# Performance work log

Hardware: AMD Instinct MI355X
Metric: run time of the kernel (lower is better)

## Reference

```python
import jax, jax.numpy as jnp
import numpy as np

H = 1024      # controller hidden size
M = 4096      # memory rows (must equal WORD per original code's buffer shapes)
WORD = 4096   # word size
R = 4         # read heads
NW = 2        # write heads
MODES = 1 + 2 * NW
EPS = 1e-3


def _lin(x, W, b):
    return x @ W.T + b


def _allocation(usage):
    # usage: [1, M] -> allocation weighting via ascending usage sort (DNC)
    u = EPS + (1.0 - EPS) * usage
    order = jnp.argsort(u, axis=1)                       # ascending (least used first)
    sorted_u = jnp.take_along_axis(u, order, axis=1)
    prod = jnp.cumprod(sorted_u, axis=1)
    excl = jnp.concatenate([jnp.ones((1, 1), u.dtype), prod[:, :-1]], axis=1)
    sorted_alloc = (1.0 - sorted_u) * excl
    return jnp.zeros_like(u).at[0, order[0]].set(sorted_alloc[0])


def _dnc_forward(x, memory, prev_read_weights, prev_write_weights, prev_link,
                 prev_precedence, prev_usage,
                 W_wv, b_wv, W_ev, b_ev, W_fg, b_fg, W_ag, b_ag, W_wg, b_wg,
                 W_rm, b_rm, W_wk, b_wk, W_ws, b_ws, W_rk, b_rk, W_rs, b_rs):
    # ---- read_inputs ----
    write_vector = _lin(x, W_wv, b_wv).reshape(NW, WORD)
    erase_vector = jax.nn.sigmoid(_lin(x, W_ev, b_ev)).reshape(NW, WORD)
    free_gate = jax.nn.sigmoid(_lin(x, W_fg, b_fg))          # [1,R]
    allocation_gate = jax.nn.sigmoid(_lin(x, W_ag, b_ag))    # [1,NW]
    write_gate = jax.nn.sigmoid(_lin(x, W_wg, b_wg))         # [1,NW]
    read_mode = jax.nn.sigmoid(_lin(x, W_rm, b_rm)).reshape(R, MODES)
    write_keys = jax.nn.sigmoid(_lin(x, W_wk, b_wk)).reshape(NW, WORD)
    write_strengths = _lin(x, W_ws, b_ws)                    # [1,NW]
    read_keys = _lin(x, W_rk, b_rk).reshape(R, WORD)
    read_strengths = _lin(x, W_rs, b_rs)                     # [1,R]

    # ---- usage ----
    ww_term = 1.0 - jnp.prod(prev_write_weights, axis=1)                   # [1,M]
    usage = prev_usage + (1.0 - prev_usage) * ww_term
    phi = 1.0 - jnp.prod(free_gate[..., None] * prev_read_weights, axis=1)
    usage = usage * phi

    # ---- write weights (cosine content + sequential allocation per head) ----
    dot = jnp.einsum('wd,bmd->bwm', write_keys, memory)                    # [1,NW,M]
    mem_norms = jnp.sqrt(jnp.sum(memory * memory, axis=2))                 # [1,M]
    key_norms = jnp.sqrt(jnp.sum(write_keys * write_keys, axis=1))         # [NW]
    similarity = dot / (key_norms[None, :, None] * mem_norms[:, None, :] + EPS)

    write_gates = (allocation_gate * write_gate)[..., None]                # [1,NW,1]
    ww_rows = []
    for i in range(NW):  # small fixed head loop (sequential usage dependency)
        beta = 1.0 + jax.nn.softplus(write_strengths[0, i])
        cw = jax.nn.softmax(similarity[0, i] * beta)                       # [M]
        a = _allocation(usage)                                             # [1,M]
        usage = usage + (1.0 - usage) * write_gates[:, i, :] * a
        ww_rows.append(write_gate[0, i] * (allocation_gate[0, i] * a[0]
                       + (1.0 - allocation_gate[0, i]) * cw))
    write_weights = jnp.stack(ww_rows)[None]                               # [1,NW,M]

    # ---- erase and write ----
    weighted_resets = write_weights[..., None] * erase_vector[None, :, None, :]
    reset_gate = jnp.prod(1.0 - weighted_resets, axis=1)                   # [1,M,WORD]
    new_memory = memory * reset_gate + jnp.einsum('bwm,wd->bmd', write_weights, write_vector)

    # ---- temporal linkage ----
    wi = write_weights[..., None]          # [1,NW,M,1]
    wj = write_weights[:, :, None, :]      # [1,NW,1,M]
    pj = prev_precedence[:, :, None, :]    # [1,NW,1,M]
    link = (1.0 - wi - wj) * prev_link + wi * pj
    link = link * (1.0 - jnp.eye(M, dtype=link.dtype))
    write_sum = jnp.sum(write_weights, axis=2, keepdims=True)
    precedence = (1.0 - write_sum) * prev_precedence + write_weights

    # ---- read weights ----
    rdot = jnp.einsum('rd,bmd->brm', read_keys, new_memory)
    new_mem_norms = jnp.sqrt(jnp.sum(new_memory * new_memory, axis=2))
    rkey_norms = jnp.sqrt(jnp.sum(read_keys * read_keys, axis=1))
    rsim = rdot / (rkey_norms[None, :, None] * new_mem_norms[:, None, :])  # note: no eps here (as in source)
    content_weights = jax.nn.softmax(rsim * read_strengths[0][None, :, None], axis=-1)

    expanded = jnp.broadcast_to(prev_read_weights[:, None], (1, NW, R, M))  # stack((rw,rw)) with NW=2
    fwd_w = jnp.einsum('bwrm,bwnm->brwn', expanded, link)   # rw @ link^T, permuted -> [1,R,NW,M]
    bwd_w = jnp.einsum('bwrm,bwmn->brwn', expanded, link)   # rw @ link,   permuted -> [1,R,NW,M]
    rm = read_mode[None]                                    # [1,R,MODES]
    backward_mode = rm[:, :, :NW]
    forward_mode = rm[:, :, NW:2 * NW]
    content_mode = rm[:, :, 2 * NW:]                        # [1,R,1]
    read_weights = (jnp.einsum('brw,brwm->brm', backward_mode, bwd_w)
                    + jnp.einsum('brw,brwm->brm', forward_mode, fwd_w)
                    + content_mode * content_weights)
    read_words = jnp.einsum('brm,bmd->brd', read_weights, new_memory)      # [1,R,WORD]
    return read_words, new_memory, read_weights, write_weights, link, precedence, usage


def setup_inputs() -> dict:
    key = jax.random.key(0)
    ks = jax.random.split(key, 32)
    rn = lambda i, s: jax.random.normal(ks[i], s, dtype=jnp.float32)
    ru = lambda i, s: jax.random.uniform(ks[i], s, dtype=jnp.float32)
    w = lambda i, s: rn(i, s) * 0.02
    return {
        'x': rn(0, (1, H)),
        'memory': rn(1, (1, M, WORD)),
        'prev_read_weights': ru(2, (1, R, M)),
        'prev_write_weights': ru(3, (1, NW, M)),
        'prev_link': ru(4, (1, NW, M, M)),
        'prev_precedence': ru(5, (1, NW, M)),
        'prev_usage': ru(6, (1, M)),
        'W_wv': w(7, (NW * WORD, H)), 'b_wv': jnp.zeros((NW * WORD,), jnp.float32),
        'W_ev': w(8, (NW * WORD, H)), 'b_ev': jnp.zeros((NW * WORD,), jnp.float32),
        'W_fg': w(9, (R, H)), 'b_fg': jnp.zeros((R,), jnp.float32),
        'W_ag': w(10, (NW, H)), 'b_ag': jnp.zeros((NW,), jnp.float32),
        'W_wg': w(11, (NW, H)), 'b_wg': jnp.zeros((NW,), jnp.float32),
        'W_rm': w(12, (R * MODES, H)), 'b_rm': jnp.zeros((R * MODES,), jnp.float32),
        'W_wk': w(13, (NW * WORD, H)), 'b_wk': jnp.zeros((NW * WORD,), jnp.float32),
        'W_ws': w(14, (NW, H)), 'b_ws': jnp.zeros((NW,), jnp.float32),
        'W_rk': w(15, (R * WORD, H)), 'b_rk': jnp.zeros((R * WORD,), jnp.float32),
        'W_rs': w(16, (R, H)), 'b_rs': jnp.zeros((R,), jnp.float32),
    }


def reference(x, memory, prev_read_weights, prev_write_weights, prev_link,
              prev_precedence, prev_usage,
              W_wv, b_wv, W_ev, b_ev, W_fg, b_fg, W_ag, b_ag, W_wg, b_wg,
              W_rm, b_rm, W_wk, b_wk, W_ws, b_ws, W_rk, b_rk, W_rs, b_rs):
    return _dnc_forward(x, memory, prev_read_weights, prev_write_weights, prev_link,
                        prev_precedence, prev_usage,
                        W_wv, b_wv, W_ev, b_ev, W_fg, b_fg, W_ag, b_ag, W_wg, b_wg,
                        W_rm, b_rm, W_wk, b_wk, W_ws, b_ws, W_rk, b_rk, W_rs, b_rs)
```

## Files before the change

### kernel.cpp

```cpp
#include <hip/hip_runtime.h>
#include <math.h>

#define HD 1024
#define MD 4096
#define WD 4096
#define RD 4
#define NWD 2
#define MODESD 5
#define EPSF 0.001f

#define O_WORDS 0
#define O_NM    16384
#define O_RW    16793600
#define O_WW    16809984
#define O_LINK  16818176
#define O_PREC  50372608
#define O_USAGE 50380800

#define WS_WV   0
#define WS_EV   8192
#define WS_WK   16384
#define WS_RK   24576
#define WS_FG   40960
#define WS_AG   40976
#define WS_WG   40992
#define WS_RM   41008
#define WS_WSTR 41040
#define WS_RS   41056
#define WS_KN   41072
#define WS_RKN  41088
#define WS_UPRE 41104
#define WS_SIM  45200
#define WS_RDOT 53392
#define WS_NMN  69776
#define WS_CONT 73872
#define WS_FWD  90256
#define WS_BWD  123024

__device__ __forceinline__ float waveReduceSum(float v) {
#pragma unroll
  for (int o = 32; o; o >>= 1) v += __shfl_down(v, o, 64);
  return v;
}

__global__ void gemv_kernel(const float* __restrict__ W, const float* __restrict__ b,
                            const float* __restrict__ x, float* __restrict__ out,
                            int rows, int act) {
  __shared__ float4 xs[HD / 4];
  int t = threadIdx.x;
  const float4* x4 = (const float4*)x;
  xs[t] = x4[t];
  __syncthreads();
  int wave = t >> 6, lane = t & 63;
  int row = blockIdx.x * 4 + wave;
  if (row >= rows) return;
  const float4* W4 = (const float4*)(W + (size_t)row * HD);
  float acc = 0.f;
#pragma unroll
  for (int i = 0; i < 4; ++i) {
    float4 w = W4[i * 64 + lane];
    float4 xv = xs[i * 64 + lane];
    acc += w.x * xv.x + w.y * xv.y + w.z * xv.z + w.w * xv.w;
  }
  acc = waveReduceSum(acc);
  if (lane == 0) {
    float v = acc + b[row];
    if (act) v = 1.f / (1.f + expf(-v));
    out[row] = v;
  }
}

__global__ void norms_kernel(const float* __restrict__ wk, const float* __restrict__ rk,
                             float* __restrict__ kn, float* __restrict__ rkn) {
  int v = blockIdx.x;
  const float* p = (v < 2) ? (wk + v * WD) : (rk + (v - 2) * WD);
  float s = 0.f;
  for (int d = threadIdx.x; d < WD; d += 256) { float t = p[d]; s += t * t; }
  s = waveReduceSum(s);
  __shared__ float sh[4];
  int wave = threadIdx.x >> 6, lane = threadIdx.x & 63;
  if (lane == 0) sh[wave] = s;
  __syncthreads();
  if (threadIdx.x == 0) {
    float r = sqrtf(sh[0] + sh[1] + sh[2] + sh[3]);
    if (v < 2) kn[v] = r; else rkn[v - 2] = r;
  }
}

__global__ void usage_kernel(const float* __restrict__ pusage, const float* __restrict__ pww,
                             const float* __restrict__ prw, const float* __restrict__ fg,
                             float* __restrict__ upre) {
  int m = blockIdx.x * 256 + threadIdx.x;
  float pw = 1.f;
#pragma unroll
  for (int w = 0; w < NWD; ++w) pw *= pww[w * MD + m];
  float pu = pusage[m];
  float u = pu + (1.f - pu) * (1.f - pw);
  float pr = 1.f;
#pragma unroll
  for (int r = 0; r < RD; ++r) pr *= fg[r] * prw[r * MD + m];
  upre[m] = u * (1.f - pr);
}

__global__ void sim_kernel(const float* __restrict__ mem, const float* __restrict__ wk,
                           const float* __restrict__ kn, float* __restrict__ sim) {
  int m = blockIdx.x;
  int t = threadIdx.x;
  const float4* row = (const float4*)(mem + (size_t)m * WD);
  const float4* k0 = (const float4*)wk;
  const float4* k1 = (const float4*)(wk + WD);
  float d0 = 0, d1 = 0, s = 0;
  for (int i = t; i < WD / 4; i += 256) {
    float4 v = row[i], a = k0[i], b = k1[i];
    d0 += v.x * a.x + v.y * a.y + v.z * a.z + v.w * a.w;
    d1 += v.x * b.x + v.y * b.y + v.z * b.z + v.w * b.w;
    s  += v.x * v.x + v.y * v.y + v.z * v.z + v.w * v.w;
  }
  d0 = waveReduceSum(d0); d1 = waveReduceSum(d1); s = waveReduceSum(s);
  __shared__ float sh[3][4];
  int wave = t >> 6, lane = t & 63;
  if (lane == 0) { sh[0][wave] = d0; sh[1][wave] = d1; sh[2][wave] = s; }
  __syncthreads();
  if (t == 0) {
    float D0 = sh[0][0] + sh[0][1] + sh[0][2] + sh[0][3];
    float D1 = sh[1][0] + sh[1][1] + sh[1][2] + sh[1][3];
    float S  = sh[2][0] + sh[2][1] + sh[2][2] + sh[2][3];
    float mn = sqrtf(S);
    sim[0 * MD + m] = D0 / (kn[0] * mn + EPSF);
    sim[1 * MD + m] = D1 / (kn[1] * mn + EPSF);
  }
}

__global__ __launch_bounds__(1024) void ww_kernel(
    const float* __restrict__ sim, const float* __restrict__ upre,
    const float* __restrict__ wstr, const float* __restrict__ ag,
    const float* __restrict__ wg, const float* __restrict__ pprec,
    float* __restrict__ out_ww, float* __restrict__ out_prec,
    float* __restrict__ out_usage) {
  __shared__ float u_s[MD];
  __shared__ float sv[MD];
  __shared__ unsigned short si[MD];
  __shared__ float a_s[MD];
  __shared__ float red[1024];
  int t = threadIdx.x;
  for (int m = t; m < MD; m += 1024) u_s[m] = upre[m];
  __syncthreads();

  for (int head = 0; head < NWD; ++head) {
    float beta = 1.f + log1pf(expf(wstr[head]));
    float agv = ag[head], wgv = wg[head];

    float mx = -3.4e38f;
    for (int m = t; m < MD; m += 1024) mx = fmaxf(mx, sim[head * MD + m] * beta);
    red[t] = mx; __syncthreads();
    for (int s = 512; s; s >>= 1) { if (t < s) red[t] = fmaxf(red[t], red[t + s]); __syncthreads(); }
    mx = red[0]; __syncthreads();
    float sm = 0.f;
    for (int m = t; m < MD; m += 1024) sm += expf(sim[head * MD + m] * beta - mx);
    red[t] = sm; __syncthreads();
    for (int s = 512; s; s >>= 1) { if (t < s) red[t] += red[t + s]; __syncthreads(); }
    float inv = 1.f / red[0]; __syncthreads();

    for (int m = t; m < MD; m += 1024) { sv[m] = EPSF + (1.f - EPSF) * u_s[m]; si[m] = (unsigned short)m; }
    __syncthreads();
    for (int k = 2; k <= MD; k <<= 1) {
      for (int j = k >> 1; j > 0; j >>= 1) {
        for (int i = t; i < MD; i += 1024) {
          int ixj = i ^ j;
          if (ixj > i) {
            float v1 = sv[i], v2 = sv[ixj];
            unsigned short i1 = si[i], i2 = si[ixj];
            bool gt = (v1 > v2) || (v1 == v2 && i1 > i2);
            bool up = ((i & k) == 0);
            if (gt == up) { sv[i] = v2; sv[ixj] = v1; si[i] = i2; si[ixj] = i1; }
          }
        }
        __syncthreads();
      }
    }
    float l0 = sv[t * 4 + 0], l1 = sv[t * 4 + 1], l2 = sv[t * 4 + 2], l3 = sv[t * 4 + 3];
    unsigned short s0 = si[t * 4 + 0], s1 = si[t * 4 + 1], s2 = si[t * 4 + 2], s3 = si[t * 4 + 3];
    red[t] = l0 * l1 * l2 * l3; __syncthreads();
    for (int off = 1; off < 1024; off <<= 1) {
      float val = (t >= off) ? red[t - off] : 1.f;
      __syncthreads();
      red[t] *= val;
      __syncthreads();
    }
    float carry = (t > 0) ? red[t - 1] : 1.f;
    __syncthreads();
    float e0 = carry, e1 = e0 * l0, e2 = e1 * l1, e3 = e2 * l2;
    a_s[s0] = (1.f - l0) * e0;
    a_s[s1] = (1.f - l1) * e1;
    a_s[s2] = (1.f - l2) * e2;
    a_s[s3] = (1.f - l3) * e3;
    __syncthreads();

    float agwg = agv * wgv;
    for (int m = t; m < MD; m += 1024) {
      float cwv = expf(sim[head * MD + m] * beta - mx) * inv;
      float a = a_s[m];
      float uu = u_s[m];
      u_s[m] = uu + (1.f - uu) * agwg * a;
      out_ww[head * MD + m] = wgv * (agv * a + (1.f - agv) * cwv);
    }
    __syncthreads();
  }

  for (int head = 0; head < NWD; ++head) {
    float s = 0.f;
    for (int m = t; m < MD; m += 1024) s += out_ww[head * MD + m];
    red[t] = s; __syncthreads();
    for (int ss = 512; ss; ss >>= 1) { if (t < ss) red[t] += red[t + ss]; __syncthreads(); }
    float wsum = red[0]; __syncthreads();
    for (int m = t; m < MD; m += 1024)
      out_prec[head * MD + m] = (1.f - wsum) * pprec[head * MD + m] + out_ww[head * MD + m];
  }
  for (int m = t; m < MD; m += 1024) out_usage[m] = u_s[m];
}

__global__ void newmem_kernel(const float* __restrict__ mem, const float* __restrict__ ww,
                              const float* __restrict__ ev, const float* __restrict__ wvv,
                              const float* __restrict__ rk, float* __restrict__ nm_out,
                              float* __restrict__ rdot, float* __restrict__ nmn) {
  int m = blockIdx.x;
  int t = threadIdx.x;
  float w0 = ww[m], w1 = ww[MD + m];
  const float4* row = (const float4*)(mem + (size_t)m * WD);
  const float4* e0 = (const float4*)ev;
  const float4* e1 = (const float4*)(ev + WD);
  const float4* v0 = (const float4*)wvv;
  const float4* v1 = (const float4*)(wvv + WD);
  const float4* k0 = (const float4*)rk;
  const float4* k1 = (const float4*)(rk + WD);
  const float4* k2 = (const float4*)(rk + 2 * WD);
  const float4* k3 = (const float4*)(rk + 3 * WD);
  float4* outp = (float4*)(nm_out + (size_t)m * WD);
  float r0 = 0, r1 = 0, r2 = 0, r3 = 0, s2 = 0;
  for (int i = t; i < WD / 4; i += 256) {
    float4 mv = row[i], ea = e0[i], eb = e1[i], va = v0[i], vb = v1[i];
    float4 o;
    o.x = mv.x * (1.f - w0 * ea.x) * (1.f - w1 * eb.x) + w0 * va.x + w1 * vb.x;
    o.y = mv.y * (1.f - w0 * ea.y) * (1.f - w1 * eb.y) + w0 * va.y + w1 * vb.y;
    o.z = mv.z * (1.f - w0 * ea.z) * (1.f - w1 * eb.z) + w0 * va.z + w1 * vb.z;
    o.w = mv.w * (1.f - w0 * ea.w) * (1.f - w1 * eb.w) + w0 * va.w + w1 * vb.w;
    outp[i] = o;
    float4 a = k0[i]; r0 += o.x * a.x + o.y * a.y + o.z * a.z + o.w * a.w;
    float4 b = k1[i]; r1 += o.x * b.x + o.y * b.y + o.z * b.z + o.w * b.w;
    float4 c = k2[i]; r2 += o.x * c.x + o.y * c.y + o.z * c.z + o.w * c.w;
    float4 d = k3[i]; r3 += o.x * d.x + o.y * d.y + o.z * d.z + o.w * d.w;
    s2 += o.x * o.x + o.y * o.y + o.z * o.z + o.w * o.w;
  }
  r0 = waveReduceSum(r0); r1 = waveReduceSum(r1); r2 = waveReduceSum(r2);
  r3 = waveReduceSum(r3); s2 = waveReduceSum(s2);
  __shared__ float sh[5][4];
  int wave = t >> 6, lane = t & 63;
  if (lane == 0) { sh[0][wave] = r0; sh[1][wave] = r1; sh[2][wave] = r2; sh[3][wave] = r3; sh[4][wave] = s2; }
  __syncthreads();
  if (t == 0) {
    float R0 = sh[0][0] + sh[0][1] + sh[0][2] + sh[0][3];
    float R1 = sh[1][0] + sh[1][1] + sh[1][2] + sh[1][3];
    float R2 = sh[2][0] + sh[2][1] + sh[2][2] + sh[2][3];
    float R3 = sh[3][0] + sh[3][1] + sh[3][2] + sh[3][3];
    float S  = sh[4][0] + sh[4][1] + sh[4][2] + sh[4][3];
    rdot[0 * MD + m] = R0; rdot[1 * MD + m] = R1;
    rdot[2 * MD + m] = R2; rdot[3 * MD + m] = R3;
    nmn[m] = sqrtf(S);
  }
}

__global__ void content_kernel(const float* __restrict__ rdot, const float* __restrict__ nmn,
                               const float* __restrict__ rkn, const float* __restrict__ rs,
                               float* __restrict__ cont) {
  int r = blockIdx.x;
  int t = threadIdx.x;
  __shared__ float vals[MD];
  __shared__ float red[256];
  float strength = rs[r], kn = rkn[r];
  float mx = -3.4e38f;
  for (int m = t; m < MD; m += 256) {
    float v = rdot[r * MD + m] / (kn * nmn[m]) * strength;
    vals[m] = v; mx = fmaxf(mx, v);
  }
  red[t] = mx; __syncthreads();
  for (int s = 128; s; s >>= 1) { if (t < s) red[t] = fmaxf(red[t], red[t + s]); __syncthreads(); }
  mx = red[0]; __syncthreads();
  float sm = 0.f;
  for (int m = t; m < MD; m += 256) { float e = expf(vals[m] - mx); vals[m] = e; sm += e; }
  red[t] = sm; __syncthreads();
  for (int s = 128; s; s >>= 1) { if (t < s) red[t] += red[t + s]; __syncthreads(); }
  float inv = 1.f / red[0];
  for (int m = t; m < MD; m += 256) cont[r * MD + m] = vals[m] * inv;
}

__global__ void link_kernel(const float* __restrict__ plink, const float* __restrict__ ww,
                            const float* __restrict__ pprec, const float* __restrict__ prw,
                            float* __restrict__ link_out, float* __restrict__ fwd) {
  int i = blockIdx.x;
  int w = blockIdx.y;
  int t = threadIdx.x;
  float wwi = ww[w * MD + i];
  const float4* pl = (const float4*)(plink + ((size_t)w * MD + i) * MD);
  const float4* wj = (const float4*)(ww + w * MD);
  const float4* pj = (const float4*)(pprec + w * MD);
  const float4* p0 = (const float4*)prw;
  const float4* p1 = (const float4*)(prw + MD);
  const float4* p2 = (const float4*)(prw + 2 * MD);
  const float4* p3 = (const float4*)(prw + 3 * MD);
  float4* lo = (float4*)(link_out + ((size_t)w * MD + i) * MD);
  float f0 = 0, f1 = 0, f2 = 0, f3 = 0;
  for (int c = t; c < MD / 4; c += 256) {
    float4 L = pl[c], WJ = wj[c], PJ = pj[c];
    float4 o;
    o.x = (1.f - wwi - WJ.x) * L.x + wwi * PJ.x;
    o.y = (1.f - wwi - WJ.y) * L.y + wwi * PJ.y;
    o.z = (1.f - wwi - WJ.z) * L.z + wwi * PJ.z;
    o.w = (1.f - wwi - WJ.w) * L.w + wwi * PJ.w;
    int j0 = c * 4;
    if ((unsigned)(i - j0) < 4u) ((float*)&o)[i - j0] = 0.f;
    lo[c] = o;
    float4 a = p0[c]; f0 += o.x * a.x + o.y * a.y + o.z * a.z + o.w * a.w;
    float4 b = p1[c]; f1 += o.x * b.x + o.y * b.y + o.z * b.z + o.w * b.w;
    float4 cc = p2[c]; f2 += o.x * cc.x + o.y * cc.y + o.z * cc.z + o.w * cc.w;
    float4 d = p3[c]; f3 += o.x * d.x + o.y * d.y + o.z * d.z + o.w * d.w;
  }
  f0 = waveReduceSum(f0); f1 = waveReduceSum(f1);
  f2 = waveReduceSum(f2); f3 = waveReduceSum(f3);
  __shared__ float sh[4][4];
  int wave = t >> 6, lane = t & 63;
  if (lane == 0) { sh[0][wave] = f0; sh[1][wave] = f1; sh[2][wave] = f2; sh[3][wave] = f3; }
  __syncthreads();
  if (t == 0) {
    fwd[(0 * NWD + w) * MD + i] = sh[0][0] + sh[0][1] + sh[0][2] + sh[0][3];
    fwd[(1 * NWD + w) * MD + i] = sh[1][0] + sh[1][1] + sh[1][2] + sh[1][3];
    fwd[(2 * NWD + w) * MD + i] = sh[2][0] + sh[2][1] + sh[2][2] + sh[2][3];
    fwd[(3 * NWD + w) * MD + i] = sh[3][0] + sh[3][1] + sh[3][2] + sh[3][3];
  }
}

__global__ void bwd_kernel(const float* __restrict__ link, const float* __restrict__ prw,
                           float* __restrict__ bwd) {
  int mc = blockIdx.x, jt = blockIdx.y, w = blockIdx.z;
  int j = jt * 256 + threadIdx.x;
  const float* base = link + (size_t)w * MD * MD;
  float a0 = 0, a1 = 0, a2 = 0, a3 = 0;
  int m0 = mc * 256;
  for (int m = m0; m < m0 + 256; ++m) {
    float lv = base[(size_t)m * MD + j];
    a0 += prw[m] * lv;
    a1 += prw[MD + m] * lv;
    a2 += prw[2 * MD + m] * lv;
    a3 += prw[3 * MD + m] * lv;
  }
  atomicAdd(&bwd[(0 * NWD + w) * MD + j], a0);
  atomicAdd(&bwd[(1 * NWD + w) * MD + j], a1);
  atomicAdd(&bwd[(2 * NWD + w) * MD + j], a2);
  atomicAdd(&bwd[(3 * NWD + w) * MD + j], a3);
}

__global__ void rw_kernel(const float* __restrict__ fwd, const float* __restrict__ bwd,
                          const float* __restrict__ cont, const float* __restrict__ rm,
                          float* __restrict__ out_rw) {
  int idx = blockIdx.x * 256 + threadIdx.x;
  int r = idx >> 12;
  int m = idx & (MD - 1);
  float v = rm[r * MODESD + 4] * cont[idx];
#pragma unroll
  for (int w = 0; w < NWD; ++w) {
    v += rm[r * MODESD + w] * bwd[(r * NWD + w) * MD + m];
    v += rm[r * MODESD + NWD + w] * fwd[(r * NWD + w) * MD + m];
  }
  out_rw[idx] = v;
}

__global__ void rwords_kernel(const float* __restrict__ rw, const float* __restrict__ nm,
                              float* __restrict__ out_words) {
  int mc = blockIdx.x;
  int d = blockIdx.y * 256 + threadIdx.x;
  float a0 = 0, a1 = 0, a2 = 0, a3 = 0;
  int m0 = mc * 256;
  for (int m = m0; m < m0 + 256; ++m) {
    float v = nm[(size_t)m * WD + d];
    a0 += rw[m] * v;
    a1 += rw[MD + m] * v;
    a2 += rw[2 * MD + m] * v;
    a3 += rw[3 * MD + m] * v;
  }
  atomicAdd(&out_words[d], a0);
  atomicAdd(&out_words[WD + d], a1);
  atomicAdd(&out_words[2 * WD + d], a2);
  atomicAdd(&out_words[3 * WD + d], a3);
}

extern "C" void kernel_launch(void* const* d_in, const int* in_sizes, int n_in,
                              void* d_out, int out_size, void* d_ws, size_t ws_size,
                              hipStream_t stream) {
  (void)in_sizes; (void)n_in; (void)out_size; (void)ws_size;
  const float* x      = (const float*)d_in[0];
  const float* memory = (const float*)d_in[1];
  const float* prw    = (const float*)d_in[2];
  const float* pww    = (const float*)d_in[3];
  const float* plink  = (const float*)d_in[4];
  const float* pprec  = (const float*)d_in[5];
  const float* pusage = (const float*)d_in[6];
  float* ws  = (float*)d_ws;
  float* out = (float*)d_out;

  hipMemsetAsync(ws + WS_BWD, 0, 32768 * sizeof(float), stream);
  hipMemsetAsync(out + O_WORDS, 0, 16384 * sizeof(float), stream);

  gemv_kernel<<<2048, 256, 0, stream>>>((const float*)d_in[7],  (const float*)d_in[8],  x, ws + WS_WV,   8192, 0);
  gemv_kernel<<<2048, 256, 0, stream>>>((const float*)d_in[9],  (const float*)d_in[10], x, ws + WS_EV,   8192, 1);
  gemv_kernel<<<1,    256, 0, stream>>>((const float*)d_in[11], (const float*)d_in[12], x, ws + WS_FG,      4, 1);
  gemv_kernel<<<1,    256, 0, stream>>>((const float*)d_in[13], (const float*)d_in[14], x, ws + WS_AG,      2, 1);
  gemv_kernel<<<1,    256, 0, stream>>>((const float*)d_in[15], (const float*)d_in[16], x, ws + WS_WG,      2, 1);
  gemv_kernel<<<5,    256, 0, stream>>>((const float*)d_in[17], (const float*)d_in[18], x, ws + WS_RM,     20, 1);
  gemv_kernel<<<2048, 256, 0, stream>>>((const float*)d_in[19], (const float*)d_in[20], x, ws + WS_WK,   8192, 1);
  gemv_kernel<<<1,    256, 0, stream>>>((const float*)d_in[21], (const float*)d_in[22], x, ws + WS_WSTR,    2, 0);
  gemv_kernel<<<4096, 256, 0, stream>>>((const float*)d_in[23], (const float*)d_in[24], x, ws + WS_RK,  16384, 0);
  gemv_kernel<<<1,    256, 0, stream>>>((const float*)d_in[25], (const float*)d_in[26], x, ws + WS_RS,      4, 0);

  norms_kernel<<<6, 256, 0, stream>>>(ws + WS_WK, ws + WS_RK, ws + WS_KN, ws + WS_RKN);
  usage_kernel<<<16, 256, 0, stream>>>(pusage, pww, prw, ws + WS_FG, ws + WS_UPRE);
  sim_kernel<<<4096, 256, 0, stream>>>(memory, ws + WS_WK, ws + WS_KN, ws + WS_SIM);
  ww_kernel<<<1, 1024, 0, stream>>>(ws + WS_SIM, ws + WS_UPRE, ws + WS_WSTR, ws + WS_AG,
                                    ws + WS_WG, pprec, out + O_WW, out + O_PREC, out + O_USAGE);
  newmem_kernel<<<4096, 256, 0, stream>>>(memory, out + O_WW, ws + WS_EV, ws + WS_WV,
                                          ws + WS_RK, out + O_NM, ws + WS_RDOT, ws + WS_NMN);
  content_kernel<<<4, 256, 0, stream>>>(ws + WS_RDOT, ws + WS_NMN, ws + WS_RKN, ws + WS_RS, ws + WS_CONT);
  link_kernel<<<dim3(MD, NWD), 256, 0, stream>>>(plink, out + O_WW, pprec, prw,
                                                 out + O_LINK, ws + WS_FWD);
  bwd_kernel<<<dim3(16, 16, 2), 256, 0, stream>>>(out + O_LINK, prw, ws + WS_BWD);
  rw_kernel<<<64, 256, 0, stream>>>(ws + WS_FWD, ws + WS_BWD, ws + WS_CONT, ws + WS_RM, out + O_RW);
  rwords_kernel<<<dim3(16, 16), 256, 0, stream>>>(out + O_RW, out + O_NM, out + O_WORDS);
}
```

Measured before the change: 820.1 us.

## Replace single-block bitonic-sort allocation with parallel rank-based log-sum allocation

The single-block ww_kernel, which bitonic-sorted 4096 usage values and ran a serial prefix product for each write head, is replaced by a parallel formulation. For each element, the exclusive cumulative product is computed as exp of the sum of logs of all smaller usage values, with index tie-breaking, using a 16x16 grid kernel with atomics. Content weights move to a separate 2-block kernel, and the per-head updates and precedence run in small grid kernels. The six tiny gemv launches are also merged into one kernel. This trades O(M^2) compares spread across the GPU for the serial single-block sort, and the log/exp product may differ slightly in numerics.

```diff
diff --git a/kernel.cpp b/kernel.cpp
--- a/kernel.cpp
+++ b/kernel.cpp
@@ -35,7 +35,15 @@
 #define WS_NMN  69776
 #define WS_CONT 73872
 #define WS_FWD  90256
-#define WS_BWD  123024
+#define WS_CW   123024
+#define WS_UU   131216
+#define WS_LU   135312
+#define WS_S0   139408
+#define WS_S1   143504
+#define WS_WWSUM 147600
+#define WS_BWD  147604
+#define WS_ZERO_START WS_S0
+#define WS_ZERO_COUNT (4096 + 4096 + 4 + 32768)
 
 __device__ __forceinline__ float waveReduceSum(float v) {
 #pragma unroll
@@ -70,6 +78,39 @@
   }
 }
 
+__global__ void small_gemv_kernel(const float* __restrict__ x,
+                                  const float* __restrict__ Wfg, const float* __restrict__ bfg,
+                                  const float* __restrict__ Wag, const float* __restrict__ bag,
+                                  const float* __restrict__ Wwg, const float* __restrict__ bwg,
+                                  const float* __restrict__ Wrm, const float* __restrict__ brm,
+                                  const float* __restrict__ Wws, const float* __restrict__ bws,
+                                  const float* __restrict__ Wrs, const float* __restrict__ brs,
+                                  float* __restrict__ ws) {
+  int blk = blockIdx.x;
+  const float* W; const float* b; float* out; int row; int act;
+  if (blk < 4)       { W = Wfg; b = bfg; out = ws + WS_FG;   row = blk;       act = 1; }
+  else if (blk < 6)  { W = Wag; b = bag; out = ws + WS_AG;   row = blk - 4;   act = 1; }
+  else if (blk < 8)  { W = Wwg; b = bwg; out = ws + WS_WG;   row = blk - 6;   act = 1; }
+  else if (blk < 28) { W = Wrm; b = brm; out = ws + WS_RM;   row = blk - 8;   act = 1; }
+  else if (blk < 30) { W = Wws; b = bws; out = ws + WS_WSTR; row = blk - 28;  act = 0; }
+  else               { W = Wrs; b = brs; out = ws + WS_RS;   row = blk - 30;  act = 0; }
+  int t = threadIdx.x;
+  const float4* W4 = (const float4*)(W + (size_t)row * HD);
+  const float4* x4 = (const float4*)x;
+  float4 w = W4[t], xv = x4[t];
+  float acc = w.x * xv.x + w.y * xv.y + w.z * xv.z + w.w * xv.w;
+  acc = waveReduceSum(acc);
+  __shared__ float sh[4];
+  int wave = t >> 6, lane = t & 63;
+  if (lane == 0) sh[wave] = acc;
+  __syncthreads();
+  if (t == 0) {
+    float v = sh[0] + sh[1] + sh[2] + sh[3] + b[row];
+    if (act) v = 1.f / (1.f + expf(-v));
+    out[row] = v;
+  }
+}
+
 __global__ void norms_kernel(const float* __restrict__ wk, const float* __restrict__ rk,
                              float* __restrict__ kn, float* __restrict__ rkn) {
   int v = blockIdx.x;
@@ -89,7 +130,8 @@
 
 __global__ void usage_kernel(const float* __restrict__ pusage, const float* __restrict__ pww,
                              const float* __restrict__ prw, const float* __restrict__ fg,
-                             float* __restrict__ upre) {
+                             float* __restrict__ upre, float* __restrict__ uu,
+                             float* __restrict__ lu) {
   int m = blockIdx.x * 256 + threadIdx.x;
   float pw = 1.f;
 #pragma unroll
@@ -99,7 +141,11 @@
   float pr = 1.f;
 #pragma unroll
   for (int r = 0; r < RD; ++r) pr *= fg[r] * prw[r * MD + m];
-  upre[m] = u * (1.f - pr);
+  float up = u * (1.f - pr);
+  upre[m] = up;
+  float v = EPSF + (1.f - EPSF) * up;
+  uu[m] = v;
+  lu[m] = logf(v);
 }
 
 __global__ void sim_kernel(const float* __restrict__ mem, const float* __restrict__ wk,
@@ -131,92 +177,98 @@
   }
 }
 
-__global__ __launch_bounds__(1024) void ww_kernel(
-    const float* __restrict__ sim, const float* __restrict__ upre,
-    const float* __restrict__ wstr, const float* __restrict__ ag,
-    const float* __restrict__ wg, const float* __restrict__ pprec,
-    float* __restrict__ out_ww, float* __restrict__ out_prec,
-    float* __restrict__ out_usage) {
-  __shared__ float u_s[MD];
-  __shared__ float sv[MD];
-  __shared__ unsigned short si[MD];
-  __shared__ float a_s[MD];
-  __shared__ float red[1024];
-  int t = threadIdx.x;
-  for (int m = t; m < MD; m += 1024) u_s[m] = upre[m];
-  __syncthreads();
-
-  for (int head = 0; head < NWD; ++head) {
-    float beta = 1.f + log1pf(expf(wstr[head]));
-    float agv = ag[head], wgv = wg[head];
-
-    float mx = -3.4e38f;
-    for (int m = t; m < MD; m += 1024) mx = fmaxf(mx, sim[head * MD + m] * beta);
-    red[t] = mx; __syncthreads();
-    for (int s = 512; s; s >>= 1) { if (t < s) red[t] = fmaxf(red[t], red[t + s]); __syncthreads(); }
-    mx = red[0]; __syncthreads();
-    float sm = 0.f;
-    for (int m = t; m < MD; m += 1024) sm += expf(sim[head * MD + m] * beta - mx);
-    red[t] = sm; __syncthreads();
-    for (int s = 512; s; s >>= 1) { if (t < s) red[t] += red[t + s]; __syncthreads(); }
-    float inv = 1.f / red[0]; __syncthreads();
-
-    for (int m = t; m < MD; m += 1024) { sv[m] = EPSF + (1.f - EPSF) * u_s[m]; si[m] = (unsigned short)m; }
-    __syncthreads();
-    for (int k = 2; k <= MD; k <<= 1) {
-      for (int j = k >> 1; j > 0; j >>= 1) {
-        for (int i = t; i < MD; i += 1024) {
-          int ixj = i ^ j;
-          if (ixj > i) {
-            float v1 = sv[i], v2 = sv[ixj];
-            unsigned short i1 = si[i], i2 = si[ixj];
-            bool gt = (v1 > v2) || (v1 == v2 && i1 > i2);
-            bool up = ((i & k) == 0);
-            if (gt == up) { sv[i] = v2; sv[ixj] = v1; si[i] = i2; si[ixj] = i1; }
-          }
-        }
-        __syncthreads();
-      }
-    }
-    float l0 = sv[t * 4 + 0], l1 = sv[t * 4 + 1], l2 = sv[t * 4 + 2], l3 = sv[t * 4 + 3];
-    unsigned short s0 = si[t * 4 + 0], s1 = si[t * 4 + 1], s2 = si[t * 4 + 2], s3 = si[t * 4 + 3];
-    red[t] = l0 * l1 * l2 * l3; __syncthreads();
-    for (int off = 1; off < 1024; off <<= 1) {
-      float val = (t >= off) ? red[t - off] : 1.f;
-      __syncthreads();
-      red[t] *= val;
-      __syncthreads();
-    }
-    float carry = (t > 0) ? red[t - 1] : 1.f;
-    __syncthreads();
-    float e0 = carry, e1 = e0 * l0, e2 = e1 * l1, e3 = e2 * l2;
-    a_s[s0] = (1.f - l0) * e0;
-    a_s[s1] = (1.f - l1) * e1;
-    a_s[s2] = (1.f - l2) * e2;
-    a_s[s3] = (1.f - l3) * e3;
-    __syncthreads();
-
-    float agwg = agv * wgv;
-    for (int m = t; m < MD; m += 1024) {
-      float cwv = expf(sim[head * MD + m] * beta - mx) * inv;
-      float a = a_s[m];
-      float uu = u_s[m];
-      u_s[m] = uu + (1.f - uu) * agwg * a;
-      out_ww[head * MD + m] = wgv * (agv * a + (1.f - agv) * cwv);
-    }
-    __syncthreads();
-  }
-
-  for (int head = 0; head < NWD; ++head) {
-    float s = 0.f;
-    for (int m = t; m < MD; m += 1024) s += out_ww[head * MD + m];
-    red[t] = s; __syncthreads();
-    for (int ss = 512; ss; ss >>= 1) { if (t < ss) red[t] += red[t + ss]; __syncthreads(); }
-    float wsum = red[0]; __syncthreads();
-    for (int m = t; m < MD; m += 1024)
-      out_prec[head * MD + m] = (1.f - wsum) * pprec[head * MD + m] + out_ww[head * MD + m];
-  }
-  for (int m = t; m < MD; m += 1024) out_usage[m] = u_s[m];
+__global__ void cw_kernel(const float* __restrict__ sim, const float* __restrict__ wstr,
+                          float* __restrict__ cw) {
+  int h = blockIdx.x;
+  int t = threadIdx.x;
+  __shared__ float vals[MD];
+  __shared__ float red[256];
+  float beta = 1.f + log1pf(expf(wstr[h]));
+  float mx = -3.4e38f;
+  for (int m = t; m < MD; m += 256) {
+    float v = sim[h * MD + m] * beta;
+    vals[m] = v; mx = fmaxf(mx, v);
+  }
+  red[t] = mx; __syncthreads();
+  for (int s = 128; s; s >>= 1) { if (t < s) red[t] = fmaxf(red[t], red[t + s]); __syncthreads(); }
+  mx = red[0]; __syncthreads();
+  float sm = 0.f;
+  for (int m = t; m < MD; m += 256) { float e = expf(vals[m] - mx); vals[m] = e; sm += e; }
+  red[t] = sm; __syncthreads();
+  for (int s = 128; s; s >>= 1) { if (t < s) red[t] += red[t + s]; __syncthreads(); }
+  float inv = 1.f / red[0];
+  for (int m = t; m < MD; m += 256) cw[h * MD + m] = vals[m] * inv;
+}
+
+__global__ void alloc_partial_kernel(const float* __restrict__ uu, const float* __restrict__ lu,
+                                     float* __restrict__ S) {
+  __shared__ float4 us[64], ls[64];
+  int t = threadIdx.x;
+  int j0 = blockIdx.y * 256;
+  if (t < 64) {
+    us[t] = ((const float4*)(uu + j0))[t];
+    ls[t] = ((const float4*)(lu + j0))[t];
+  }
+  __syncthreads();
+  int i = blockIdx.x * 256 + t;
+  float ui = uu[i];
+  float s = 0.f;
+#pragma unroll 4
+  for (int c = 0; c < 64; ++c) {
+    float4 u4 = us[c], l4 = ls[c];
+    int jb = j0 + c * 4;
+    s += ((u4.x < ui) || (u4.x == ui && (jb + 0) < i)) ? l4.x : 0.f;
+    s += ((u4.y < ui) || (u4.y == ui && (jb + 1) < i)) ? l4.y : 0.f;
+    s += ((u4.z < ui) || (u4.z == ui && (jb + 2) < i)) ? l4.z : 0.f;
+    s += ((u4.w < ui) || (u4.w == ui && (jb + 3) < i)) ? l4.w : 0.f;
+  }
+  atomicAdd(&S[i], s);
+}
+
+__global__ void update0_kernel(const float* __restrict__ S0, const float* __restrict__ cw,
+                               const float* __restrict__ ag, const float* __restrict__ wg,
+                               const float* __restrict__ upre, float* __restrict__ uu,
+                               float* __restrict__ lu, float* __restrict__ u1,
+                               float* __restrict__ out_ww, float* __restrict__ wwsum) {
+  int m = blockIdx.x * 256 + threadIdx.x;
+  float agv = ag[0], wgv = wg[0];
+  float uum = uu[m];
+  float a = (1.f - uum) * expf(S0[m]);
+  float w = wgv * (agv * a + (1.f - agv) * cw[m]);
+  out_ww[m] = w;
+  float up = upre[m];
+  float un = up + (1.f - up) * (agv * wgv) * a;
+  u1[m] = un;
+  float v = EPSF + (1.f - EPSF) * un;
+  uu[m] = v;
+  lu[m] = logf(v);
+  float p = waveReduceSum(w);
+  if ((threadIdx.x & 63) == 0) atomicAdd(&wwsum[0], p);
+}
+
+__global__ void update1_kernel(const float* __restrict__ S1, const float* __restrict__ cw,
+                               const float* __restrict__ ag, const float* __restrict__ wg,
+                               const float* __restrict__ u1, const float* __restrict__ uu,
+                               float* __restrict__ out_ww, float* __restrict__ out_usage,
+                               float* __restrict__ wwsum) {
+  int m = blockIdx.x * 256 + threadIdx.x;
+  float agv = ag[1], wgv = wg[1];
+  float uum = uu[m];
+  float a = (1.f - uum) * expf(S1[m]);
+  float w = wgv * (agv * a + (1.f - agv) * cw[MD + m]);
+  out_ww[MD + m] = w;
+  float un = u1[m];
+  out_usage[m] = un + (1.f - un) * (agv * wgv) * a;
+  float p = waveReduceSum(w);
+  if ((threadIdx.x & 63) == 0) atomicAdd(&wwsum[1], p);
+}
+
+__global__ void prec_kernel(const float* __restrict__ ww, const float* __restrict__ wwsum,
+                            const float* __restrict__ pprec, float* __restrict__ out_prec) {
+  int m = blockIdx.x * 256 + threadIdx.x;
+  float s0 = wwsum[0], s1 = wwsum[1];
+  out_prec[m] = (1.f - s0) * pprec[m] + ww[m];
+  out_prec[MD + m] = (1.f - s1) * pprec[MD + m] + ww[MD + m];
 }
 
 __global__ void newmem_kernel(const float* __restrict__ mem, const float* __restrict__ ww,
@@ -258,14 +310,11 @@
   if (lane == 0) { sh[0][wave] = r0; sh[1][wave] = r1; sh[2][wave] = r2; sh[3][wave] = r3; sh[4][wave] = s2; }
   __syncthreads();
   if (t == 0) {
-    float R0 = sh[0][0] + sh[0][1] + sh[0][2] + sh[0][3];
-    float R1 = sh[1][0] + sh[1][1] + sh[1][2] + sh[1][3];
-    float R2 = sh[2][0] + sh[2][1] + sh[2][2] + sh[2][3];
-    float R3 = sh[3][0] + sh[3][1] + sh[3][2] + sh[3][3];
-    float S  = sh[4][0] + sh[4][1] + sh[4][2] + sh[4][3];
-    rdot[0 * MD + m] = R0; rdot[1 * MD + m] = R1;
-    rdot[2 * MD + m] = R2; rdot[3 * MD + m] = R3;
-    nmn[m] = sqrtf(S);
+    rdot[0 * MD + m] = sh[0][0] + sh[0][1] + sh[0][2] + sh[0][3];
+    rdot[1 * MD + m] = sh[1][0] + sh[1][1] + sh[1][2] + sh[1][3];
+    rdot[2 * MD + m] = sh[2][0] + sh[2][1] + sh[2][2] + sh[2][3];
+    rdot[3 * MD + m] = sh[3][0] + sh[3][1] + sh[3][2] + sh[3][3];
+    nmn[m] = sqrtf(sh[4][0] + sh[4][1] + sh[4][2] + sh[4][3]);
   }
 }
 
@@ -406,25 +455,37 @@
   float* ws  = (float*)d_ws;
   float* out = (float*)d_out;
 
-  hipMemsetAsync(ws + WS_BWD, 0, 32768 * sizeof(float), stream);
+  hipMemsetAsync(ws + WS_ZERO_START, 0, WS_ZERO_COUNT * sizeof(float), stream);
   hipMemsetAsync(out + O_WORDS, 0, 16384 * sizeof(float), stream);
 
-  gemv_kernel<<<2048, 256, 0, stream>>>((const float*)d_in[7],  (const float*)d_in[8],  x, ws + WS_WV,   8192, 0);
-  gemv_kernel<<<2048, 256, 0, stream>>>((const float*)d_in[9],  (const float*)d_in[10], x, ws + WS_EV,   8192, 1);
-  gemv_kernel<<<1,    256, 0, stream>>>((const float*)d_in[11], (const float*)d_in[12], x, ws + WS_FG,      4, 1);
-  gemv_kernel<<<1,    256, 0, stream>>>((const float*)d_in[13], (const float*)d_in[14], x, ws + WS_AG,      2, 1);
-  gemv_kernel<<<1,    256, 0, stream>>>((const float*)d_in[15], (const float*)d_in[16], x, ws + WS_WG,      2, 1);
-  gemv_kernel<<<5,    256, 0, stream>>>((const float*)d_in[17], (const float*)d_in[18], x, ws + WS_RM,     20, 1);
-  gemv_kernel<<<2048, 256, 0, stream>>>((const float*)d_in[19], (const float*)d_in[20], x, ws + WS_WK,   8192, 1);
-  gemv_kernel<<<1,    256, 0, stream>>>((const float*)d_in[21], (const float*)d_in[22], x, ws + WS_WSTR,    2, 0);
-  gemv_kernel<<<4096, 256, 0, stream>>>((const float*)d_in[23], (const float*)d_in[24], x, ws + WS_RK,  16384, 0);
-  gemv_kernel<<<1,    256, 0, stream>>>((const float*)d_in[25], (const float*)d_in[26], x, ws + WS_RS,      4, 0);
+  gemv_kernel<<<2048, 256, 0, stream>>>((const float*)d_in[7],  (const float*)d_in[8],  x, ws + WS_WV, 8192, 0);
+  gemv_kernel<<<2048, 256, 0, stream>>>((const float*)d_in[9],  (const float*)d_in[10], x, ws + WS_EV, 8192, 1);
+  gemv_kernel<<<2048, 256, 0, stream>>>((const float*)d_in[19], (const float*)d_in[20], x, ws + WS_WK, 8192, 1);
+  gemv_kernel<<<4096, 256, 0, stream>>>((const float*)d_in[23], (const float*)d_in[24], x, ws + WS_RK, 16384, 0);
+  small_gemv_kernel<<<34, 256, 0, stream>>>(x,
+      (const float*)d_in[11], (const float*)d_in[12],
+      (const float*)d_in[13], (const float*)d_in[14],
+      (const float*)d_in[15], (const float*)d_in[16],
+      (const float*)d_in[17], (const float*)d_in[18],
+      (const float*)d_in[21], (const float*)d_in[22],
+      (const float*)d_in[25], (const float*)d_in[26],
+      ws);
 
   norms_kernel<<<6, 256, 0, stream>>>(ws + WS_WK, ws + WS_RK, ws + WS_KN, ws + WS_RKN);
-  usage_kernel<<<16, 256, 0, stream>>>(pusage, pww, prw, ws + WS_FG, ws + WS_UPRE);
+  usage_kernel<<<16, 256, 0, stream>>>(pusage, pww, prw, ws + WS_FG, ws + WS_UPRE, ws + WS_UU, ws + WS_LU);
   sim_kernel<<<4096, 256, 0, stream>>>(memory, ws + WS_WK, ws + WS_KN, ws + WS_SIM);
-  ww_kernel<<<1, 1024, 0, stream>>>(ws + WS_SIM, ws + WS_UPRE, ws + WS_WSTR, ws + WS_AG,
-                                    ws + WS_WG, pprec, out + O_WW, out + O_PREC, out + O_USAGE);
+  cw_kernel<<<2, 256, 0, stream>>>(ws + WS_SIM, ws + WS_WSTR, ws + WS_CW);
+
+  alloc_partial_kernel<<<dim3(16, 16), 256, 0, stream>>>(ws + WS_UU, ws + WS_LU, ws + WS_S0);
+  update0_kernel<<<16, 256, 0, stream>>>(ws + WS_S0, ws + WS_CW, ws + WS_AG, ws + WS_WG,
+                                         ws + WS_UPRE, ws + WS_UU, ws + WS_LU, ws + WS_UPRE,
+                                         out + O_WW, ws + WS_WWSUM);
+  alloc_partial_kernel<<<dim3(16, 16), 256, 0, stream>>>(ws + WS_UU, ws + WS_LU, ws + WS_S1);
+  update1_kernel<<<16, 256, 0, stream>>>(ws + WS_S1, ws + WS_CW, ws + WS_AG, ws + WS_WG,
+                                         ws + WS_UPRE, ws + WS_UU, out + O_WW, out + O_USAGE,
+                                         ws + WS_WWSUM);
+  prec_kernel<<<16, 256, 0, stream>>>(out + O_WW, ws + WS_WWSUM, pprec, out + O_PREC);
+
   newmem_kernel<<<4096, 256, 0, stream>>>(memory, out + O_WW, ws + WS_EV, ws + WS_WV,
                                           ws + WS_RK, out + O_NM, ws + WS_RDOT, ws + WS_NMN);
   content_kernel<<<4, 256, 0, stream>>>(ws + WS_RDOT, ws + WS_NMN, ws + WS_RKN, ws + WS_RS, ws + WS_CONT);
```

Measured after the change: 690.6 us. 1.19x faster.
